# Performance work log

Hardware: AMD Instinct MI355X
Metric: run time of the kernel (lower is better)

## Reference

```python
import jax, jax.numpy as jnp
import numpy as np

B, C, H, W = 8, 256, 64, 64
NH = 8            # num_heads
OC = 256          # out_channels
D = C // NH       # per-head channel dim = 32
HW = H * W
BN_EPS = 1e-5


def _conv1x1(x, Wt, b):
    # x: [B,Cin,H,W], Wt: [Cout,Cin]
    return jnp.einsum('bchw,oc->bohw', x, Wt) + b[None, :, None, None]


def setup_inputs() -> dict:
    key = jax.random.key(0)
    ks = jax.random.split(key, 16)
    def n(k, shape, s=0.05):
        return jax.random.normal(k, shape, dtype=jnp.float32) * s
    return {
        'F1': jax.random.normal(ks[0], (B, C, H, W), jnp.float32),
        'F2': jax.random.normal(ks[1], (B, C, H, W), jnp.float32),
        'Wq':  n(ks[2], (C, 2 * C)), 'bq':  n(ks[3], (C,)),
        'Wk1': n(ks[4], (C, C)),     'bk1': n(ks[5], (C,)),
        'Wv1': n(ks[6], (C, C)),     'bv1': n(ks[7], (C,)),
        'Wk2': n(ks[8], (C, C)),     'bk2': n(ks[9], (C,)),
        'Wv2': n(ks[10], (C, C)),    'bv2': n(ks[11], (C,)),
        'mu':  jnp.full((1,), 0.5, jnp.float32),   # learnable scalar (init 0 in torch; nonzero here for nontrivial math)
        'Wc':  n(ks[12], (OC, 2 * C, 3, 3)),
        'gamma': jnp.ones((OC,), jnp.float32),
        'beta':  jnp.zeros((OC,), jnp.float32),
        'rmean': jnp.zeros((OC,), jnp.float32),
        'rvar':  jnp.ones((OC,), jnp.float32),
    }


def reference(F1, F2, Wq, bq, Wk1, bk1, Wv1, bv1, Wk2, bk2, Wv2, bv2,
              mu, Wc, gamma, beta, rmean, rvar):
    # fused query from both streams
    Qf = _conv1x1(jnp.concatenate([F1, F2], axis=1), Wq, bq)          # [B,C,H,W]
    Q = Qf.reshape(B, NH, D, HW).transpose(0, 1, 3, 2)                # [B,h,HW,d]
    Qs = jax.nn.softmax(Q, axis=-1)                                   # softmax over d

    def branch(F, Wk, bk, Wv, bv):
        K = _conv1x1(F, Wk, bk).reshape(B, NH, D, HW)                 # [B,h,d,HW]
        V = _conv1x1(F, Wv, bv).reshape(B, NH, D, HW)                 # [B,h,d,HW]
        Ks = jax.nn.softmax(K, axis=-1)                               # softmax over HW
        Att = jnp.einsum('bhdn,bhne->bhde', Ks, Qs)                   # [B,h,d,d]
        Xw = jnp.einsum('bhde,bhen->bhdn', Att, V)                    # [B,h,d,HW]
        return Xw.reshape(B, C, H, W)

    X1 = branch(F1, Wk1, bk1, Wv1, bv1)
    X2 = branch(F2, Wk2, bk2, Wv2, bv2)

    fused = jnp.concatenate([mu * X1 + F1, mu * X2 + F2], axis=1)     # [B,2C,H,W]
    y = jax.lax.conv_general_dilated(
        fused, Wc, window_strides=(1, 1), padding='SAME',
        dimension_numbers=('NCHW', 'OIHW', 'NCHW'))                   # [B,OC,H,W]
    # inference-mode BatchNorm + ReLU
    inv = gamma / jnp.sqrt(rvar + BN_EPS)
    y = y * inv[None, :, None, None] + (beta - rmean * inv)[None, :, None, None]
    return jax.nn.relu(y)
```

## Files before the change

kernel.cpp:

```cpp
#include <hip/hip_runtime.h>

typedef __attribute__((ext_vector_type(8))) short bf8;
typedef __attribute__((ext_vector_type(4))) float f32x4;

static __device__ __forceinline__ unsigned short f2b(float x) {
    unsigned u = __builtin_bit_cast(unsigned, x);
    u += 0x7fffu + ((u >> 16) & 1u);
    return (unsigned short)(u >> 16);
}

static __device__ __forceinline__ void gload_lds16(const void* g, void* l) {
    __builtin_amdgcn_global_load_lds(
        (const __attribute__((address_space(1))) unsigned int*)g,
        (__attribute__((address_space(3))) unsigned int*)l, 16, 0, 0);
}

__global__ __launch_bounds__(256) void k_prep(
    const float* __restrict__ Wq, const float* __restrict__ Wk1, const float* __restrict__ Wv1,
    const float* __restrict__ Wk2, const float* __restrict__ Wv2, const float* __restrict__ Wc,
    const float* __restrict__ gamma, const float* __restrict__ beta,
    const float* __restrict__ rmean, const float* __restrict__ rvar,
    const float* __restrict__ F1, const float* __restrict__ F2,
    unsigned short* __restrict__ WQB, unsigned short* __restrict__ WKB, unsigned short* __restrict__ WVB,
    unsigned short* __restrict__ WCB, float* __restrict__ BNS, float* __restrict__ BNB,
    float* __restrict__ SUMK, unsigned short* __restrict__ XT)
{
    const int bid = blockIdx.x;
    if (bid < 4096) {
        __shared__ float tile[64][65];
        const int b = bid >> 9;
        const int c0 = ((bid >> 6) & 7) * 64;
        const int p0 = (bid & 63) * 64;
        const int tx = threadIdx.x & 63;
        const int ty = threadIdx.x >> 6;
        const float* src = (c0 < 256) ? F1 : F2;
        const int cb = c0 & 255;
#pragma unroll
        for (int i = 0; i < 16; i++) {
            int cl = i * 4 + ty;
            tile[cl][tx] = src[((size_t)b * 256 + cb + cl) * 4096 + p0 + tx];
        }
        __syncthreads();
        const int t = threadIdx.x;
        const int p = t >> 2;
        const int cg = (t & 3) * 16;
        unsigned short tmp[16];
#pragma unroll
        for (int j = 0; j < 16; j++) tmp[j] = f2b(tile[cg + j][p]);
        unsigned short* dst = XT + ((size_t)b * 4096 + p0 + p) * 512 + c0 + cg;
        *(uint4*)dst = *(const uint4*)tmp;
        *(uint4*)(dst + 8) = *(const uint4*)(tmp + 8);
        return;
    }
    const int total = 131072 + 4 * 65536 + 1179648 + 256 + 4096;
    for (int i = (bid - 4096) * 256 + threadIdx.x; i < total; i += 256 * 256) {
        int j = i;
        if (j < 131072) { WQB[j] = f2b(Wq[j]); continue; }
        j -= 131072;
        if (j < 65536) { WKB[j] = f2b(Wk1[j]); continue; }
        j -= 65536;
        if (j < 65536) { WKB[65536 + j] = f2b(Wk2[j]); continue; }
        j -= 65536;
        if (j < 65536) { WVB[j] = f2b(Wv1[j]); continue; }
        j -= 65536;
        if (j < 65536) { WVB[65536 + j] = f2b(Wv2[j]); continue; }
        j -= 65536;
        if (j < 1179648) {
            int cl = j & 63;
            int rest = j >> 6;
            int o = rest & 255;
            int tc = rest >> 8;
            int tap = tc >> 3, ccb = tc & 7;
            int c = ccb * 64 + cl;
            WCB[j] = f2b(Wc[(size_t)(o * 512 + c) * 9 + tap]);
            continue;
        }
        j -= 1179648;
        if (j < 256) {
            float inv = gamma[j] * rsqrtf(rvar[j] + 1e-5f);
            BNS[j] = inv;
            BNB[j] = beta[j] - rmean[j] * inv;
            continue;
        }
        j -= 256;
        SUMK[j] = 0.0f;
    }
}

template<int MODE>
__global__ __launch_bounds__(256) void k_gemm1x1(
    const unsigned short* __restrict__ A,
    const unsigned short* __restrict__ XT,
    const float* __restrict__ bias,
    const float* __restrict__ bias2,
    unsigned short* __restrict__ outU,
    float* __restrict__ outF,
    const unsigned short* __restrict__ QSp,
    float* __restrict__ ATTP,
    int Kd)
{
    __shared__ unsigned short lds[2][2][128 * 64];
    int br = 0, b = blockIdx.z, myy = blockIdx.y;
    if (MODE == 3) { br = blockIdx.z >> 3; b = blockIdx.z & 7; }
    if (MODE == 4) { br = blockIdx.y >> 1; myy = blockIdx.y & 1; }
    const int m0 = myy * 128;
    const int n0 = blockIdx.x * 128;
    const int co = (MODE == 2) ? 0 : br * 256;
    const unsigned short* Ab = A + (size_t)br * 65536;
    const float* bi = br ? bias2 : bias;
    const int lane = threadIdx.x & 63;
    const int wv = threadIdx.x >> 6;
    const int wr = wv >> 1, wc = wv & 1;
    const int lrow = lane & 15, kg = lane >> 4;
    const int px = lane >> 3, sl = lane & 7;
    const int nt = Kd >> 6;

    f32x4 acc[4][4];
#pragma unroll
    for (int mi = 0; mi < 4; mi++)
#pragma unroll
        for (int ni = 0; ni < 4; ni++)
            acc[mi][ni] = (f32x4){0.f, 0.f, 0.f, 0.f};

#pragma unroll
    for (int j = 0; j < 4; j++) {
        int r0 = wv * 32 + j * 8;
        gload_lds16(Ab + (size_t)(m0 + r0 + px) * Kd + (sl ^ px) * 8, &lds[0][0][r0 * 64]);
        gload_lds16(XT + ((size_t)b * 4096 + n0 + r0 + px) * 512 + co + (sl ^ px) * 8, &lds[0][1][r0 * 64]);
    }
    __syncthreads();

    int cb = 0;
    for (int kt = 0; kt < nt; kt++) {
        if (kt + 1 < nt) {
            int k0 = (kt + 1) << 6;
            int nb = cb ^ 1;
#pragma unroll
            for (int j = 0; j < 4; j++) {
                int r0 = wv * 32 + j * 8;
                gload_lds16(Ab + (size_t)(m0 + r0 + px) * Kd + k0 + (sl ^ px) * 8, &lds[nb][0][r0 * 64]);
                gload_lds16(XT + ((size_t)b * 4096 + n0 + r0 + px) * 512 + co + k0 + (sl ^ px) * 8, &lds[nb][1][r0 * 64]);
            }
        }
        const unsigned short* wa = lds[cb][0];
        const unsigned short* wb = lds[cb][1];
#pragma unroll
        for (int klo = 0; klo < 64; klo += 32) {
            const int slin = klo >> 3;
            bf8 a[4], bv[4];
#pragma unroll
            for (int mi = 0; mi < 4; mi++) {
                int ol = wr * 64 + mi * 16 + lrow;
                a[mi] = *(const bf8*)(wa + ol * 64 + (((slin + kg) ^ (ol & 7)) * 8));
            }
#pragma unroll
            for (int ni = 0; ni < 4; ni++) {
                int nl = wc * 64 + ni * 16 + lrow;
                bv[ni] = *(const bf8*)(wb + nl * 64 + (((slin + kg) ^ (nl & 7)) * 8));
            }
#pragma unroll
            for (int mi = 0; mi < 4; mi++)
#pragma unroll
                for (int ni = 0; ni < 4; ni++)
                    acc[mi][ni] = __builtin_amdgcn_mfma_f32_16x16x32_bf16(a[mi], bv[ni], acc[mi][ni], 0, 0, 0);
        }
        __syncthreads();
        cb ^= 1;
    }

    if (MODE == 2) {
#pragma unroll
        for (int hh = 0; hh < 2; hh++) {
            float vv[2][4][4];
            float mx[4];
#pragma unroll
            for (int ni = 0; ni < 4; ni++) mx[ni] = -1e30f;
#pragma unroll
            for (int ms = 0; ms < 2; ms++) {
                int mi = hh * 2 + ms;
                int row0 = m0 + wr * 64 + mi * 16 + kg * 4;
#pragma unroll
                for (int r = 0; r < 4; r++) {
                    float bb = bi[row0 + r];
#pragma unroll
                    for (int ni = 0; ni < 4; ni++) {
                        float x = acc[mi][ni][r] + bb;
                        vv[ms][r][ni] = x;
                        mx[ni] = fmaxf(mx[ni], x);
                    }
                }
            }
#pragma unroll
            for (int ni = 0; ni < 4; ni++) {
                mx[ni] = fmaxf(mx[ni], __shfl_xor(mx[ni], 16, 64));
                mx[ni] = fmaxf(mx[ni], __shfl_xor(mx[ni], 32, 64));
            }
            float sm[4] = {0.f, 0.f, 0.f, 0.f};
#pragma unroll
            for (int ms = 0; ms < 2; ms++)
#pragma unroll
                for (int r = 0; r < 4; r++)
#pragma unroll
                    for (int ni = 0; ni < 4; ni++) {
                        float e = __expf(vv[ms][r][ni] - mx[ni]);
                        vv[ms][r][ni] = e;
                        sm[ni] += e;
                    }
#pragma unroll
            for (int ni = 0; ni < 4; ni++) {
                sm[ni] += __shfl_xor(sm[ni], 16, 64);
                sm[ni] += __shfl_xor(sm[ni], 32, 64);
                sm[ni] = 1.0f / sm[ni];
            }
            int h = (m0 + wr * 64 + hh * 32) >> 5;
#pragma unroll
            for (int ms = 0; ms < 2; ms++) {
                int e0 = ms * 16 + kg * 4;
#pragma unroll
                for (int r = 0; r < 4; r++)
#pragma unroll
                    for (int ni = 0; ni < 4; ni++) {
                        int col = n0 + wc * 64 + ni * 16 + lrow;
                        outU[((size_t)(b * 8 + h) * 32 + e0 + r) * 4096 + col] = f2b(vv[ms][r][ni] * sm[ni]);
                    }
            }
        }
    } else if (MODE == 3) {
        unsigned short* P = &lds[0][0][0];
        float* red = (float*)&lds[1][0][0];
        float ps[4][4];
#pragma unroll
        for (int mi = 0; mi < 4; mi++) {
            int rowl0 = wr * 64 + mi * 16 + kg * 4;
#pragma unroll
            for (int r = 0; r < 4; r++) {
                float bb = bi[m0 + rowl0 + r];
                int row = rowl0 + r;
                float s = 0.f;
#pragma unroll
                for (int ni = 0; ni < 4; ni++) {
                    float e = __expf(acc[mi][ni][r] + bb);
                    int col = wc * 64 + ni * 16 + lrow;
                    int slot = (col >> 3) ^ (row & 7);
                    P[row * 128 + slot * 8 + (col & 7)] = f2b(e);
                    s += e;
                }
                ps[mi][r] = s;
            }
        }
#pragma unroll
        for (int mi = 0; mi < 4; mi++)
#pragma unroll
            for (int r = 0; r < 4; r++)
                red[(wr * 64 + mi * 16 + kg * 4 + r) * 33 + wc * 16 + lrow] = ps[mi][r];
        __syncthreads();
        if (threadIdx.x < 128) {
            float s = 0.f;
#pragma unroll
            for (int j = 0; j < 32; j++) s += red[threadIdx.x * 33 + j];
            atomicAdd(&outF[br * 2048 + b * 256 + m0 + threadIdx.x], s);
        }
        const int hh = wv;
        const int bh = b * 8 + (m0 >> 5) + hh;
        const unsigned short* QSb = QSp + ((size_t)bh * 32) * 4096 + n0;
        f32x4 acc2[2][2];
#pragma unroll
        for (int mi2 = 0; mi2 < 2; mi2++)
#pragma unroll
            for (int ni2 = 0; ni2 < 2; ni2++)
                acc2[mi2][ni2] = (f32x4){0.f, 0.f, 0.f, 0.f};
#pragma unroll
        for (int ks = 0; ks < 4; ks++) {
            bf8 pa[2], qb[2];
#pragma unroll
            for (int mi2 = 0; mi2 < 2; mi2++) {
                int row = hh * 32 + mi2 * 16 + lrow;
                int slot = (ks * 4 + kg) ^ (row & 7);
                pa[mi2] = *(const bf8*)(P + row * 128 + slot * 8);
            }
#pragma unroll
            for (int ni2 = 0; ni2 < 2; ni2++)
                qb[ni2] = *(const bf8*)(QSb + (size_t)(ni2 * 16 + lrow) * 4096 + ks * 32 + kg * 8);
#pragma unroll
            for (int mi2 = 0; mi2 < 2; mi2++)
#pragma unroll
                for (int ni2 = 0; ni2 < 2; ni2++)
                    acc2[mi2][ni2] = __builtin_amdgcn_mfma_f32_16x16x32_bf16(pa[mi2], qb[ni2], acc2[mi2][ni2], 0, 0, 0);
        }
        float* dst = ATTP + (size_t)br * 2097152 + ((size_t)bh * 32 + (n0 >> 7)) * 1024;
#pragma unroll
        for (int mi2 = 0; mi2 < 2; mi2++)
#pragma unroll
            for (int ni2 = 0; ni2 < 2; ni2++)
#pragma unroll
                for (int r = 0; r < 4; r++)
                    dst[(mi2 * 16 + kg * 4 + r) * 32 + ni2 * 16 + lrow] = acc2[mi2][ni2][r];
    } else {
        unsigned short* vlds = &lds[0][0][0];
#pragma unroll
        for (int mi = 0; mi < 4; mi++) {
#pragma unroll
            for (int ni = 0; ni < 4; ni++) {
                int ch0 = wr * 64 + mi * 16 + kg * 4;
                int p = wc * 64 + ni * 16 + lrow;
                int sg = ch0 >> 3;
                unsigned long long pk = 0;
#pragma unroll
                for (int r = 0; r < 4; r++) {
                    unsigned short us = f2b(acc[mi][ni][r] + bi[m0 + ch0 + r]);
                    pk |= (unsigned long long)us << (16 * r);
                }
                *(unsigned long long*)(vlds + p * 128 + ((sg ^ (p & 15)) * 8) + (ch0 & 7)) = pk;
            }
        }
        __syncthreads();
        const int hl = wv;
        const int bh = b * 8 + (m0 >> 5) + hl;
        const unsigned short* ATTh = QSp + (size_t)br * 65536 + (size_t)bh * 1024;
        bf8 af[2];
#pragma unroll
        for (int mi2 = 0; mi2 < 2; mi2++)
            af[mi2] = *(const bf8*)(ATTh + (mi2 * 16 + lrow) * 32 + kg * 8);
#pragma unroll
        for (int ni2 = 0; ni2 < 8; ni2++) {
            int pp = ni2 * 16 + lrow;
            bf8 bf = *(const bf8*)(vlds + pp * 128 + (((hl * 4 + kg) ^ (pp & 15)) * 8));
            f32x4 pa0 = (f32x4){0.f, 0.f, 0.f, 0.f};
            f32x4 pa1 = (f32x4){0.f, 0.f, 0.f, 0.f};
            pa0 = __builtin_amdgcn_mfma_f32_16x16x32_bf16(af[0], bf, pa0, 0, 0, 0);
            pa1 = __builtin_amdgcn_mfma_f32_16x16x32_bf16(af[1], bf, pa1, 0, 0, 0);
#pragma unroll
            for (int mi2 = 0; mi2 < 2; mi2++) {
                f32x4 pa = mi2 ? pa1 : pa0;
                int c0 = co + m0 + hl * 32 + mi2 * 16 + kg * 4;
                size_t base = ((size_t)b * 4096 + n0 + pp) * 512 + c0;
                unsigned long long rin = *(const unsigned long long*)(XT + base);
                unsigned long long pk = 0;
#pragma unroll
                for (int r = 0; r < 4; r++) {
                    unsigned short us = (unsigned short)(rin >> (16 * r));
                    float f = __builtin_bit_cast(float, ((unsigned)us) << 16);
                    pk |= (unsigned long long)f2b(pa[r] + f) << (16 * r);
                }
                *(unsigned long long*)(outU + base) = pk;
            }
        }
    }
}

__global__ __launch_bounds__(256) void k_att_red(const float* __restrict__ ATTP,
                                                 const float* __restrict__ SUMK,
                                                 const float* __restrict__ mup,
                                                 unsigned short* __restrict__ ATT)
{
    const int gid = blockIdx.x;
    const int br = gid >> 6, bh = gid & 63;
    const int b = bh >> 3, h = bh & 7;
    const int tid = threadIdx.x;
    const float mu = mup[0];
    const float* src = ATTP + (size_t)br * 2097152;
#pragma unroll
    for (int i = 0; i < 4; i++) {
        int idx = tid + i * 256;
        int d = idx >> 5;
        float s = 0.f;
        for (int nch = 0; nch < 32; nch++)
            s += src[((size_t)bh * 32 + nch) * 1024 + idx];
        ATT[(size_t)br * 65536 + (size_t)bh * 1024 + idx] = f2b(mu * s / SUMK[br * 2048 + b * 256 + h * 32 + d]);
    }
}

__global__ __launch_bounds__(256) void k_conv3(
    const unsigned short* __restrict__ WB2,
    const unsigned short* __restrict__ FUSED,
    const float* __restrict__ BNS, const float* __restrict__ BNB,
    float* __restrict__ out)
{
    __shared__ unsigned short lds_in[4 * 72 * 64];
    __shared__ unsigned short lds_w[2][128 * 64];

    const int b = blockIdx.z;
    const int m0 = blockIdx.y * 128;
    const int ry = blockIdx.x;
    const int lane = threadIdx.x & 63;
    const int wv = threadIdx.x >> 6;
    const int wr = wv >> 1, wc = wv & 1;
    const int lrow = lane & 15, kg = lane >> 4;
    const int px = lane >> 3, sl = lane & 7;

    f32x4 acc[4][4];
#pragma unroll
    for (int mi = 0; mi < 4; mi++)
#pragma unroll
        for (int ni = 0; ni < 4; ni++)
            acc[mi][ni] = (f32x4){0.f, 0.f, 0.f, 0.f};

    for (int ccb = 0; ccb < 8; ccb++) {
        for (int u = wv; u < 36; u += 4) {
            int rl = u / 9, seg = u - rl * 9;
            int gy = ry * 2 + rl - 1;
            bool rowok = ((unsigned)gy < 64u);
            int xi0 = seg * 8;
            unsigned short* ldsb = lds_in + (rl * 72 + xi0) * 64;
            int x = xi0 + px - 4;
            const unsigned short* src = FUSED
                + ((size_t)(b * 4096 + gy * 64 + x)) * 512 + ccb * 64 + (sl ^ px) * 8;
            if (rowok && seg >= 1 && seg <= 7) {
                gload_lds16(src, ldsb);
            } else {
                uint4 v = {0u, 0u, 0u, 0u};
                if (rowok && ((unsigned)x < 64u)) v = *(const uint4*)src;
                *(uint4*)(ldsb + lane * 8) = v;
            }
        }
        {
            const unsigned short* base = WB2 + (((size_t)(0 * 8 + ccb) * 256) + m0) * 64;
#pragma unroll
            for (int jw = 0; jw < 4; jw++) {
                int o0 = wv * 32 + jw * 8;
                gload_lds16(base + (size_t)(o0 + px) * 64 + (sl ^ px) * 8, &lds_w[0][o0 * 64]);
            }
        }
        __syncthreads();

        for (int tap = 0; tap < 9; tap++) {
            if (tap < 8) {
                const unsigned short* base = WB2 + (((size_t)((tap + 1) * 8 + ccb) * 256) + m0) * 64;
                unsigned short* wdst = lds_w[(tap + 1) & 1];
#pragma unroll
                for (int jw = 0; jw < 4; jw++) {
                    int o0 = wv * 32 + jw * 8;
                    gload_lds16(base + (size_t)(o0 + px) * 64 + (sl ^ px) * 8, &wdst[o0 * 64]);
                }
            }
            const unsigned short* wb = lds_w[tap & 1];
            const int ky = tap / 3, kx = tap - ky * 3;
            const int rl = wc + ky;
#pragma unroll
            for (int k0 = 0; k0 < 64; k0 += 32) {
                const int slin = k0 >> 3;
                bf8 a[4], bv[4];
#pragma unroll
                for (int mi = 0; mi < 4; mi++) {
                    int ol = wr * 64 + mi * 16 + lrow;
                    int s = (slin + kg) ^ (ol & 7);
                    a[mi] = *(const bf8*)(wb + ol * 64 + s * 8);
                }
#pragma unroll
                for (int ni = 0; ni < 4; ni++) {
                    int xi = ni * 16 + lrow + kx + 3;
                    int s = (slin + kg) ^ (xi & 7);
                    bv[ni] = *(const bf8*)(lds_in + (rl * 72 + xi) * 64 + s * 8);
                }
                __builtin_amdgcn_s_setprio(1);
#pragma unroll
                for (int mi = 0; mi < 4; mi++)
#pragma unroll
                    for (int ni = 0; ni < 4; ni++)
                        acc[mi][ni] = __builtin_amdgcn_mfma_f32_16x16x32_bf16(a[mi], bv[ni], acc[mi][ni], 0, 0, 0);
                __builtin_amdgcn_s_setprio(0);
            }
            __syncthreads();
        }
    }

#pragma unroll
    for (int mi = 0; mi < 4; mi++) {
#pragma unroll
        for (int ni = 0; ni < 4; ni++) {
            int o0 = m0 + wr * 64 + mi * 16 + kg * 4;
            int p = (ry * 2 + wc) * 64 + ni * 16 + lrow;
#pragma unroll
            for (int r = 0; r < 4; r++) {
                int o = o0 + r;
                float v = acc[mi][ni][r] * BNS[o] + BNB[o];
                out[((size_t)b * 256 + o) * 4096 + p] = fmaxf(v, 0.0f);
            }
        }
    }
}

extern "C" void kernel_launch(void* const* d_in, const int* in_sizes, int n_in,
                              void* d_out, int out_size, void* d_ws, size_t ws_size,
                              hipStream_t stream)
{
    (void)in_sizes; (void)n_in; (void)out_size; (void)ws_size;
    const float* F1 = (const float*)d_in[0];
    const float* F2 = (const float*)d_in[1];
    const float* Wq = (const float*)d_in[2];
    const float* bq = (const float*)d_in[3];
    const float* Wk1 = (const float*)d_in[4];
    const float* bk1 = (const float*)d_in[5];
    const float* Wv1 = (const float*)d_in[6];
    const float* bv1 = (const float*)d_in[7];
    const float* Wk2 = (const float*)d_in[8];
    const float* bk2 = (const float*)d_in[9];
    const float* Wv2 = (const float*)d_in[10];
    const float* bv2 = (const float*)d_in[11];
    const float* mu = (const float*)d_in[12];
    const float* Wc = (const float*)d_in[13];
    const float* gamma = (const float*)d_in[14];
    const float* beta = (const float*)d_in[15];
    const float* rmean = (const float*)d_in[16];
    const float* rvar = (const float*)d_in[17];

    char* ws = (char*)d_ws;
    size_t off = 0;
    auto give = [&](size_t bytes) -> char* {
        char* p = ws + off;
        off = (off + bytes + 255) & ~(size_t)255;
        return p;
    };
    unsigned short* XT     = (unsigned short*)give(33554432);
    unsigned short* FUSED2 = (unsigned short*)give(33554432);
    unsigned short* QS  = (unsigned short*)give(16777216);
    unsigned short* WQB = (unsigned short*)give(262144);
    unsigned short* WKB = (unsigned short*)give(262144);
    unsigned short* WVB = (unsigned short*)give(262144);
    unsigned short* WCB = (unsigned short*)give(2359296);
    unsigned short* ATT = (unsigned short*)give(262144);
    float* BNS = (float*)give(1024);
    float* BNB = (float*)give(1024);
    float* ATTP = (float*)give(16777216);
    float* SUMK = (float*)give(16384);

    k_prep<<<4352, 256, 0, stream>>>(Wq, Wk1, Wv1, Wk2, Wv2, Wc, gamma, beta, rmean, rvar,
                                     F1, F2, WQB, WKB, WVB, WCB, BNS, BNB, SUMK, XT);
    k_gemm1x1<2><<<dim3(32, 2, 8), 256, 0, stream>>>(WQB, XT, bq, nullptr, QS, nullptr, nullptr, nullptr, 512);
    k_gemm1x1<3><<<dim3(32, 2, 16), 256, 0, stream>>>(WKB, XT, bk1, bk2, nullptr, SUMK, QS, ATTP, 256);
    k_att_red<<<128, 256, 0, stream>>>(ATTP, SUMK, mu, ATT);
    k_gemm1x1<4><<<dim3(32, 4, 8), 256, 0, stream>>>(WVB, XT, bv1, bv2, FUSED2, nullptr, ATT, nullptr, 256);
    k_conv3<<<dim3(32, 2, 8), 256, 0, stream>>>(WCB, FUSED2, BNS, BNB, (float*)d_out);
}
```

Measured before the change: 176.5 us.

## Rotate MODE-4 K-tile order, reuse residual from LDS, vectorize attention reduce

In MODE 4 of the GEMM kernel the K-tile loop now starts at an offset chosen per block and wraps around, so the last tile left in LDS holds the residual input slice. The epilogue reads the residual from that LDS buffer rather than reloading it from global memory, and the V tile is laid out in two 64-pixel halves to fit around it. The attention partial-sum reduction now uses float4 loads and packed bf16 stores, and the setprio hints around the MFMA block in the 3x3 conv are removed. These are separate ideas, and the residual reuse relies on the exact LDS buffer layout being right.

Measured after the change: 171.3 us, median of 3. 1.03x faster.

```diff
diff --git a/kernel.cpp b/kernel.cpp
--- a/kernel.cpp
+++ b/kernel.cpp
@@ -114,6 +114,7 @@
     const int lrow = lane & 15, kg = lane >> 4;
     const int px = lane >> 3, sl = lane & 7;
     const int nt = Kd >> 6;
+    const int kts = (MODE == 4) ? (((m0 >> 6) + 2) & 3) : 0;
 
     f32x4 acc[4][4];
 #pragma unroll
@@ -122,18 +123,21 @@
         for (int ni = 0; ni < 4; ni++)
             acc[mi][ni] = (f32x4){0.f, 0.f, 0.f, 0.f};
 
-#pragma unroll
-    for (int j = 0; j < 4; j++) {
-        int r0 = wv * 32 + j * 8;
-        gload_lds16(Ab + (size_t)(m0 + r0 + px) * Kd + (sl ^ px) * 8, &lds[0][0][r0 * 64]);
-        gload_lds16(XT + ((size_t)b * 4096 + n0 + r0 + px) * 512 + co + (sl ^ px) * 8, &lds[0][1][r0 * 64]);
+    {
+        int k0p = kts << 6;
+#pragma unroll
+        for (int j = 0; j < 4; j++) {
+            int r0 = wv * 32 + j * 8;
+            gload_lds16(Ab + (size_t)(m0 + r0 + px) * Kd + k0p + (sl ^ px) * 8, &lds[0][0][r0 * 64]);
+            gload_lds16(XT + ((size_t)b * 4096 + n0 + r0 + px) * 512 + co + k0p + (sl ^ px) * 8, &lds[0][1][r0 * 64]);
+        }
     }
     __syncthreads();
 
     int cb = 0;
     for (int kt = 0; kt < nt; kt++) {
         if (kt + 1 < nt) {
-            int k0 = (kt + 1) << 6;
+            int k0 = (MODE == 4) ? (((kts + kt + 1) & 3) << 6) : ((kt + 1) << 6);
             int nb = cb ^ 1;
 #pragma unroll
             for (int j = 0; j < 4; j++) {
@@ -296,7 +300,7 @@
                 for (int r = 0; r < 4; r++)
                     dst[(mi2 * 16 + kg * 4 + r) * 32 + ni2 * 16 + lrow] = acc2[mi2][ni2][r];
     } else {
-        unsigned short* vlds = &lds[0][0][0];
+        unsigned short* L = &lds[0][0][0];
 #pragma unroll
         for (int mi = 0; mi < 4; mi++) {
 #pragma unroll
@@ -310,7 +314,7 @@
                     unsigned short us = f2b(acc[mi][ni][r] + bi[m0 + ch0 + r]);
                     pk |= (unsigned long long)us << (16 * r);
                 }
-                *(unsigned long long*)(vlds + p * 128 + ((sg ^ (p & 15)) * 8) + (ch0 & 7)) = pk;
+                *(unsigned long long*)(L + wc * 16384 + (p & 63) * 128 + ((sg ^ (p & 15)) * 8) + (ch0 & 7)) = pk;
             }
         }
         __syncthreads();
@@ -324,7 +328,7 @@
 #pragma unroll
         for (int ni2 = 0; ni2 < 8; ni2++) {
             int pp = ni2 * 16 + lrow;
-            bf8 bf = *(const bf8*)(vlds + pp * 128 + (((hl * 4 + kg) ^ (pp & 15)) * 8));
+            const bf8 bf = *(const bf8*)(L + (ni2 >> 2) * 16384 + (pp & 63) * 128 + (((hl * 4 + kg) ^ (pp & 15)) * 8));
             f32x4 pa0 = (f32x4){0.f, 0.f, 0.f, 0.f};
             f32x4 pa1 = (f32x4){0.f, 0.f, 0.f, 0.f};
             pa0 = __builtin_amdgcn_mfma_f32_16x16x32_bf16(af[0], bf, pa0, 0, 0, 0);
@@ -332,9 +336,14 @@
 #pragma unroll
             for (int mi2 = 0; mi2 < 2; mi2++) {
                 f32x4 pa = mi2 ? pa1 : pa0;
-                int c0 = co + m0 + hl * 32 + mi2 * 16 + kg * 4;
+                int cl = hl * 32 + mi2 * 16 + kg * 4;
+                int buf = cl >> 6;
+                int jj = cl & 63;
+                int slot = (jj >> 3) ^ (pp & 7);
+                unsigned long long rin = *(const unsigned long long*)
+                    (L + buf * 16384 + 8192 + pp * 64 + slot * 8 + (jj & 7));
+                int c0 = co + m0 + cl;
                 size_t base = ((size_t)b * 4096 + n0 + pp) * 512 + c0;
-                unsigned long long rin = *(const unsigned long long*)(XT + base);
                 unsigned long long pk = 0;
 #pragma unroll
                 for (int r = 0; r < 4; r++) {
@@ -358,16 +367,20 @@
     const int b = bh >> 3, h = bh & 7;
     const int tid = threadIdx.x;
     const float mu = mup[0];
-    const float* src = ATTP + (size_t)br * 2097152;
-#pragma unroll
-    for (int i = 0; i < 4; i++) {
-        int idx = tid + i * 256;
-        int d = idx >> 5;
-        float s = 0.f;
-        for (int nch = 0; nch < 32; nch++)
-            s += src[((size_t)bh * 32 + nch) * 1024 + idx];
-        ATT[(size_t)br * 65536 + (size_t)bh * 1024 + idx] = f2b(mu * s / SUMK[br * 2048 + b * 256 + h * 32 + d]);
-    }
+    const float* src = ATTP + (size_t)br * 2097152 + (size_t)bh * 32768;
+    const int idx = tid * 4;
+    const int d = idx >> 5;
+    float4 s = {0.f, 0.f, 0.f, 0.f};
+    for (int nch = 0; nch < 32; nch++) {
+        float4 v = *(const float4*)&src[nch * 1024 + idx];
+        s.x += v.x; s.y += v.y; s.z += v.z; s.w += v.w;
+    }
+    float inv = mu / SUMK[br * 2048 + b * 256 + h * 32 + d];
+    unsigned long long pk = (unsigned long long)f2b(s.x * inv)
+        | ((unsigned long long)f2b(s.y * inv) << 16)
+        | ((unsigned long long)f2b(s.z * inv) << 32)
+        | ((unsigned long long)f2b(s.w * inv) << 48);
+    *(unsigned long long*)(ATT + (size_t)br * 65536 + (size_t)bh * 1024 + idx) = pk;
 }
 
 __global__ __launch_bounds__(256) void k_conv3(
@@ -452,13 +465,11 @@
                     int s = (slin + kg) ^ (xi & 7);
                     bv[ni] = *(const bf8*)(lds_in + (rl * 72 + xi) * 64 + s * 8);
                 }
-                __builtin_amdgcn_s_setprio(1);
 #pragma unroll
                 for (int mi = 0; mi < 4; mi++)
 #pragma unroll
                     for (int ni = 0; ni < 4; ni++)
                         acc[mi][ni] = __builtin_amdgcn_mfma_f32_16x16x32_bf16(a[mi], bv[ni], acc[mi][ni], 0, 0, 0);
-                __builtin_amdgcn_s_setprio(0);
             }
             __syncthreads();
         }
```
